# Optimization experiments

Hardware: AMD Instinct MI355X
Metric: run time of the kernel (lower is better)

The kernel has to match this reference:

```python
import jax, jax.numpy as jnp
import numpy as np

B, L, D, H = 2, 2048, 2048, 16
HD = D // H  # 128, must be even for RoPE


def rope(x, seq_len, theta=10000.0):
    """Apply RoPE to x of shape [B, H, L, Dh]."""
    d = x.shape[-1]
    freqs = 1.0 / theta ** (jnp.arange(0, d, 2, dtype=x.dtype) / d)  # [d/2]
    t = jnp.arange(seq_len, dtype=x.dtype)
    f = jnp.outer(t, freqs)                      # [L, d/2]
    sin = jnp.repeat(jnp.sin(f), 2, axis=-1)     # [L, d]
    cos = jnp.repeat(jnp.cos(f), 2, axis=-1)
    x1, x2 = x[..., ::2], x[..., 1::2]
    x_rot = jnp.stack([-x2, x1], axis=-1).reshape(x.shape)
    return x * cos + x_rot * sin


def setup_inputs() -> dict:
    key = jax.random.key(0)
    k1, k2, k3 = jax.random.split(key, 3)
    x = jax.random.normal(k1, (B, L, D), dtype=jnp.float32)
    w_qkv = jax.random.normal(k2, (D, 3 * D), dtype=jnp.float32) * (1.0 / np.sqrt(D))
    w_proj = jax.random.normal(k3, (D, D), dtype=jnp.float32) * (1.0 / np.sqrt(D))
    return {"x": x, "w_qkv": w_qkv, "w_proj": w_proj}


def reference(x, w_qkv, w_proj):
    Bc, Lc, Dc = x.shape
    scale = 1.0 / np.sqrt(HD)
    qkv = (x @ w_qkv).reshape(Bc, Lc, 3, H, HD)
    q, k, v = qkv[:, :, 0], qkv[:, :, 1], qkv[:, :, 2]   # [B, L, H, Dh]
    # transpose to [B, H, L, Dh], then RoPE (position axis = L)
    q = rope(jnp.transpose(q, (0, 2, 1, 3)), Lc)
    k = rope(jnp.transpose(k, (0, 2, 1, 3)), Lc)
    v = jnp.transpose(v, (0, 2, 1, 3))
    att = jnp.einsum("bhqd,bhkd->bhqk", q, k) * scale   # [B, H, L, L]
    att = jax.nn.softmax(att, axis=-1)
    out = jnp.einsum("bhqk,bhkd->bhqd", att, v)          # [B, H, L, Dh]
    out = jnp.transpose(out, (0, 2, 1, 3)).reshape(Bc, Lc, Dc)
    return out @ w_proj
```

## Files before the change

### kernel.cpp

```cpp
#include <hip/hip_runtime.h>
#include <hip/hip_bf16.h>
#include <cstdint>

typedef short short8 __attribute__((ext_vector_type(8)));
typedef float f32x4 __attribute__((ext_vector_type(4)));

#define AS1 __attribute__((address_space(1)))
#define AS3 __attribute__((address_space(3)))

static __device__ __forceinline__ void async_cp16(const void* g, void* l) {
  __builtin_amdgcn_global_load_lds((const AS1 unsigned int*)g, (AS3 unsigned int*)l, 16, 0, 0);
}

static __device__ __forceinline__ ushort f2bf(float f) {
  unsigned u = __builtin_bit_cast(unsigned, f);
  u += 0x7fffu + ((u >> 16) & 1u);
  return (ushort)(u >> 16);
}
static __device__ __forceinline__ float bf2f(ushort h) {
  unsigned u = ((unsigned)h) << 16;
  return __builtin_bit_cast(float, u);
}

__global__ void cvt_bf16_kernel(const float* __restrict__ in, ushort* __restrict__ out, int n4) {
  int i = blockIdx.x * blockDim.x + threadIdx.x;
  if (i >= n4) return;
  float4 v = ((const float4*)in)[i];
  ushort4 o;
  o.x = f2bf(v.x); o.y = f2bf(v.y); o.z = f2bf(v.z); o.w = f2bf(v.w);
  ((ushort4*)out)[i] = o;
}

__global__ void transpose_cvt_kernel(const float* __restrict__ in, ushort* __restrict__ out,
                                     int R, int C) {
  __shared__ ushort tile[32][33];
  int c0 = blockIdx.x * 32, r0 = blockIdx.y * 32;
  int tx = threadIdx.x, ty = threadIdx.y;
  for (int j = 0; j < 32; j += 8)
    tile[ty + j][tx] = f2bf(in[(size_t)(r0 + ty + j) * C + c0 + tx]);
  __syncthreads();
  for (int j = 0; j < 32; j += 8)
    out[(size_t)(c0 + ty + j) * R + r0 + tx] = tile[tx][ty + j];
}

__global__ __launch_bounds__(256) void gemm_qkv_kernel(
    const ushort* __restrict__ A, const ushort* __restrict__ Bt,
    ushort* __restrict__ qr, ushort* __restrict__ kr, ushort* __restrict__ vt,
    int K, int N) {
  __shared__ __align__(16) ushort smem[8192];
  ushort* As = smem;
  ushort* Bs = smem + 4096;
  const int tid = threadIdx.x;
  const int wave = tid >> 6, lane = tid & 63;
  const int wr = (wave >> 1) * 64, wc = (wave & 1) * 64;
  const int m0 = blockIdx.y * 128, n0 = blockIdx.x * 128;
  const int l4 = lane >> 2, lb8 = (lane & 3) * 8;
  const int fr = lane & 15, fq8 = (lane >> 4) * 8;

  f32x4 acc[4][4] = {};

  for (int k0 = 0; k0 < K; k0 += 32) {
#pragma unroll
    for (int j = 0; j < 2; ++j) {
      const int r = wave * 32 + j * 16 + l4;
      async_cp16(A + (size_t)(m0 + r) * K + k0 + lb8, As + wave * 1024 + j * 512);
      async_cp16(Bt + (size_t)(n0 + r) * K + k0 + lb8, Bs + wave * 1024 + j * 512);
    }
    __syncthreads();
    short8 af[4], bf_[4];
#pragma unroll
    for (int i = 0; i < 4; ++i) {
      af[i] = *(const short8*)(As + (wr + i * 16 + fr) * 32 + fq8);
      bf_[i] = *(const short8*)(Bs + (wc + i * 16 + fr) * 32 + fq8);
    }
#pragma unroll
    for (int mi = 0; mi < 4; ++mi)
#pragma unroll
      for (int ni = 0; ni < 4; ++ni)
        acc[mi][ni] = __builtin_amdgcn_mfma_f32_16x16x32_bf16(af[mi], bf_[ni], acc[mi][ni], 0, 0, 0);
    __syncthreads();
  }

  const int rq = (lane >> 4) * 4;
  if (n0 >= 4096) {
    ushort* vtile = smem + wave * 1024;
    const int col0 = n0 + wc;
    const int row0 = m0 + wr;
    const int b = row0 >> 11, l0 = row0 & 2047;
    const int swz = (fr & 3) << 4;
#pragma unroll
    for (int ni = 0; ni < 4; ++ni) {
#pragma unroll
      for (int mi = 0; mi < 4; ++mi)
#pragma unroll
        for (int r = 0; r < 4; ++r) {
          int ll = mi * 16 + rq + r;
          vtile[fr * 64 + (ll ^ swz)] = f2bf(acc[mi][ni][r]);
        }
#pragma unroll
      for (int t = 0; t < 2; ++t) {
        int dl = t * 8 + (lane >> 3);
        int l8 = (lane & 7) * 8;
        int lsw = l8 ^ ((dl & 3) << 4);
        int rem = (col0 + ni * 16 + dl) & 2047;
        int h = rem >> 7, dh = rem & 127;
        *(short8*)(vt + ((size_t)((b << 4) + h) * 128 + dh) * 2048 + l0 + l8) =
            *(const short8*)(vtile + dl * 64 + lsw);
      }
    }
  } else {
    ushort* dst = (n0 >= 2048) ? kr : qr;
#pragma unroll
    for (int mi = 0; mi < 4; ++mi)
#pragma unroll
      for (int ni = 0; ni < 4; ++ni) {
        int col = n0 + wc + ni * 16 + fr;
        int rem = col & 2047, h = rem >> 7, dh = rem & 127;
#pragma unroll
        for (int r = 0; r < 4; ++r) {
          int row = m0 + wr + mi * 16 + rq + r;
          int b = row >> 11, l = row & 2047;
          dst[((size_t)((b << 4) + h) * 2048 + l) * 128 + dh] = f2bf(acc[mi][ni][r]);
        }
      }
  }
}

__global__ __launch_bounds__(256) void gemm_out_kernel(
    const ushort* __restrict__ A, const ushort* __restrict__ Bt,
    float* __restrict__ C, int K, int N) {
  __shared__ __align__(16) ushort As[128 * 32];
  __shared__ __align__(16) ushort Bs[128 * 32];
  const int tid = threadIdx.x;
  const int wave = tid >> 6, lane = tid & 63;
  const int wr = (wave >> 1) * 64, wc = (wave & 1) * 64;
  const int m0 = blockIdx.y * 128, n0 = blockIdx.x * 128;
  const int l4 = lane >> 2, lb8 = (lane & 3) * 8;
  const int fr = lane & 15, fq8 = (lane >> 4) * 8;

  f32x4 acc[4][4] = {};

  for (int k0 = 0; k0 < K; k0 += 32) {
#pragma unroll
    for (int j = 0; j < 2; ++j) {
      const int r = wave * 32 + j * 16 + l4;
      async_cp16(A + (size_t)(m0 + r) * K + k0 + lb8, As + wave * 1024 + j * 512);
      async_cp16(Bt + (size_t)(n0 + r) * K + k0 + lb8, Bs + wave * 1024 + j * 512);
    }
    __syncthreads();
    short8 af[4], bf_[4];
#pragma unroll
    for (int i = 0; i < 4; ++i) {
      af[i] = *(const short8*)(As + (wr + i * 16 + fr) * 32 + fq8);
      bf_[i] = *(const short8*)(Bs + (wc + i * 16 + fr) * 32 + fq8);
    }
#pragma unroll
    for (int mi = 0; mi < 4; ++mi)
#pragma unroll
      for (int ni = 0; ni < 4; ++ni)
        acc[mi][ni] = __builtin_amdgcn_mfma_f32_16x16x32_bf16(af[mi], bf_[ni], acc[mi][ni], 0, 0, 0);
    __syncthreads();
  }

  const int rq = (lane >> 4) * 4;
#pragma unroll
  for (int mi = 0; mi < 4; ++mi)
#pragma unroll
    for (int ni = 0; ni < 4; ++ni) {
      int col = n0 + wc + ni * 16 + fr;
#pragma unroll
      for (int r = 0; r < 4; ++r) {
        int row = m0 + wr + mi * 16 + rq + r;
        C[(size_t)row * N + col] = acc[mi][ni][r];
      }
    }
}

__global__ void rope_kernel(ushort* __restrict__ q, ushort* __restrict__ k) {
  int idx = blockIdx.x * 256 + threadIdx.x;
  int i = idx & 63;
  int l = (idx >> 6) & 2047;
  int bh = idx >> 17;
  float inv = __builtin_amdgcn_exp2f(-(float)i * (13.287712379549449f / 64.0f));
  float f = (float)l * inv;
  float s, c;
  sincosf(f, &s, &c);
  size_t base = ((size_t)bh * 2048 + l) * 128 + 2 * i;
  float q0 = bf2f(q[base]), q1 = bf2f(q[base + 1]);
  q[base] = f2bf(q0 * c - q1 * s);
  q[base + 1] = f2bf(q1 * c + q0 * s);
  float k0 = bf2f(k[base]), k1 = bf2f(k[base + 1]);
  k[base] = f2bf(k0 * c - k1 * s);
  k[base + 1] = f2bf(k1 * c + k0 * s);
}

__global__ __launch_bounds__(512, 4) void flash_kernel(
    const ushort* __restrict__ qr, const ushort* __restrict__ kr,
    const ushort* __restrict__ vtg, ushort* __restrict__ att) {
  __shared__ __align__(16) ushort Ks[64 * 136];
  __shared__ __align__(16) ushort Vt[128 * 68];
  __shared__ __align__(16) ushort Ps[8 * 16 * 68];

  const int tid = threadIdx.x;
  const int wave = tid >> 6, lane = tid & 63;
  const int qt = blockIdx.x & 15;
  const int bh = blockIdx.x >> 4;
  const int q0 = qt * 128 + wave * 16;
  const size_t bh_base = (size_t)bh * 2048 * 128;

  const int fr = lane & 15;
  const int fq = lane >> 4;
  const float cs = 0.08838834764831845f * 1.4426950408889634f;

  short8 qf[4];
  {
    const ushort* qp = qr + bh_base + (size_t)(q0 + fr) * 128 + fq * 8;
#pragma unroll
    for (int kc = 0; kc < 4; ++kc) qf[kc] = *(const short8*)(qp + kc * 32);
  }

  f32x4 oacc[8];
#pragma unroll
  for (int i = 0; i < 8; ++i) oacc[i] = (f32x4){0.f, 0.f, 0.f, 0.f};
  float l_r[4] = {0.f, 0.f, 0.f, 0.f};

  const int krow = tid >> 3;
  const int kc8 = tid & 7;
  const int vrow = tid >> 2;
  const int vc8 = tid & 3;

  ushort* pw = &Ps[wave * 16 * 68];

  short8 kpre[2], vpre[2];
  {
    const ushort* kg = kr + bh_base + (size_t)krow * 128;
    const ushort* vg = vtg + bh_base + (size_t)vrow * 2048;
#pragma unroll
    for (int i = 0; i < 2; ++i) {
      kpre[i] = *(const short8*)(kg + (kc8 + 8 * i) * 8);
      vpre[i] = *(const short8*)(vg + (vc8 + 4 * i) * 8);
    }
  }

  for (int kt = 0; kt < 32; ++kt) {
    __syncthreads();
#pragma unroll
    for (int i = 0; i < 2; ++i) {
      *(short8*)(&Ks[krow * 136 + (kc8 + 8 * i) * 8]) = kpre[i];
      *(short8*)(&Vt[vrow * 68 + (vc8 + 4 * i) * 8]) = vpre[i];
    }
    __syncthreads();
    if (kt < 31) {
      const ushort* kg = kr + bh_base + (size_t)((kt + 1) * 64 + krow) * 128;
      const ushort* vg = vtg + bh_base + (size_t)vrow * 2048 + (kt + 1) * 64;
#pragma unroll
      for (int i = 0; i < 2; ++i) {
        kpre[i] = *(const short8*)(kg + (kc8 + 8 * i) * 8);
        vpre[i] = *(const short8*)(vg + (vc8 + 4 * i) * 8);
      }
    }

    float sv[4][4];
#pragma unroll
    for (int nt = 0; nt < 4; ++nt) {
      f32x4 a = (f32x4){0.f, 0.f, 0.f, 0.f};
#pragma unroll
      for (int kc = 0; kc < 4; ++kc) {
        short8 kf = *(const short8*)(&Ks[(nt * 16 + fr) * 136 + kc * 32 + fq * 8]);
        a = __builtin_amdgcn_mfma_f32_16x16x32_bf16(qf[kc], kf, a, 0, 0, 0);
      }
#pragma unroll
      for (int r = 0; r < 4; ++r) sv[nt][r] = a[r];
    }

#pragma unroll
    for (int nt = 0; nt < 4; ++nt)
#pragma unroll
      for (int r = 0; r < 4; ++r) {
        float pv = __builtin_amdgcn_exp2f(sv[nt][r] * cs);
        l_r[r] += pv;
        pw[(fq * 4 + r) * 68 + nt * 16 + fr] = f2bf(pv);
      }

#pragma unroll
    for (int kc2 = 0; kc2 < 2; ++kc2) {
      short8 pf = *(const short8*)(&pw[fr * 68 + kc2 * 32 + fq * 8]);
#pragma unroll
      for (int dt = 0; dt < 8; ++dt) {
        short8 vf = *(const short8*)(&Vt[(dt * 16 + fr) * 68 + kc2 * 32 + fq * 8]);
        oacc[dt] = __builtin_amdgcn_mfma_f32_16x16x32_bf16(pf, vf, oacc[dt], 0, 0, 0);
      }
    }
  }

  const int b = bh >> 4, h = bh & 15;
#pragma unroll
  for (int r = 0; r < 4; ++r) {
    float l = l_r[r];
    l += __shfl_xor(l, 1);
    l += __shfl_xor(l, 2);
    l += __shfl_xor(l, 4);
    l += __shfl_xor(l, 8);
    float inv = 1.0f / l;
    size_t row = (size_t)(b * 2048 + q0 + fq * 4 + r) * 2048 + h * 128;
#pragma unroll
    for (int dt = 0; dt < 8; ++dt)
      att[row + dt * 16 + fr] = f2bf(oacc[dt][r] * inv);
  }
}

extern "C" void kernel_launch(void* const* d_in, const int* in_sizes, int n_in,
                              void* d_out, int out_size, void* d_ws, size_t ws_size,
                              hipStream_t stream) {
  const float* x = (const float*)d_in[0];
  const float* w_qkv = (const float*)d_in[1];
  const float* w_proj = (const float*)d_in[2];
  float* out = (float*)d_out;

  char* p = (char*)d_ws;
  ushort* xb = (ushort*)p;  p += (size_t)4096 * 2048 * 2;
  ushort* wqt = (ushort*)p; p += (size_t)6144 * 2048 * 2;
  ushort* wpt = (ushort*)p; p += (size_t)2048 * 2048 * 2;
  ushort* qr = (ushort*)p;  p += (size_t)32 * 2048 * 128 * 2;
  ushort* kr = (ushort*)p;  p += (size_t)32 * 2048 * 128 * 2;
  ushort* vt = (ushort*)p;  p += (size_t)32 * 2048 * 128 * 2;
  ushort* att = (ushort*)p; p += (size_t)4096 * 2048 * 2;

  cvt_bf16_kernel<<<8192, 256, 0, stream>>>(x, xb, 4096 * 2048 / 4);
  transpose_cvt_kernel<<<dim3(192, 64), dim3(32, 8), 0, stream>>>(w_qkv, wqt, 2048, 6144);
  transpose_cvt_kernel<<<dim3(64, 64), dim3(32, 8), 0, stream>>>(w_proj, wpt, 2048, 2048);
  gemm_qkv_kernel<<<dim3(48, 32), 256, 0, stream>>>(xb, wqt, qr, kr, vt, 2048, 6144);
  rope_kernel<<<16384, 256, 0, stream>>>(qr, kr);
  flash_kernel<<<512, 512, 0, stream>>>(qr, kr, vt, att);
  gemm_out_kernel<<<dim3(16, 32), 256, 0, stream>>>(att, wpt, out, 2048, 2048);
}
```

Measured before the change: 462.4 us.

## Rewrite QKV GEMM with 256x256 tiles and double-buffered k64 pipeline

```diff
diff --git a/kernel.cpp b/kernel.cpp
--- a/kernel.cpp
+++ b/kernel.cpp
@@ -21,6 +21,11 @@
   unsigned u = ((unsigned)h) << 16;
   return __builtin_bit_cast(float, u);
 }
+
+#define FENCE asm volatile("" ::: "memory")
+#define BARRIER do { FENCE; __builtin_amdgcn_s_barrier(); FENCE; } while (0)
+#define WAITLGKM asm volatile("s_waitcnt lgkmcnt(0)" ::: "memory")
+#define WAITVM(N) asm volatile("s_waitcnt vmcnt(" #N ")" ::: "memory")
 
 __global__ void cvt_bf16_kernel(const float* __restrict__ in, ushort* __restrict__ out, int n4) {
   int i = blockIdx.x * blockDim.x + threadIdx.x;
@@ -43,84 +48,153 @@
     out[(size_t)(c0 + ty + j) * R + r0 + tx] = tile[tx][ty + j];
 }
 
-__global__ __launch_bounds__(256) void gemm_qkv_kernel(
+__global__ __launch_bounds__(512, 2) void gemm_qkv_kernel(
     const ushort* __restrict__ A, const ushort* __restrict__ Bt,
     ushort* __restrict__ qr, ushort* __restrict__ kr, ushort* __restrict__ vt,
     int K, int N) {
-  __shared__ __align__(16) ushort smem[8192];
-  ushort* As = smem;
-  ushort* Bs = smem + 4096;
+  __shared__ __align__(16) ushort smem[65536];
   const int tid = threadIdx.x;
   const int wave = tid >> 6, lane = tid & 63;
-  const int wr = (wave >> 1) * 64, wc = (wave & 1) * 64;
-  const int m0 = blockIdx.y * 128, n0 = blockIdx.x * 128;
-  const int l4 = lane >> 2, lb8 = (lane & 3) * 8;
-  const int fr = lane & 15, fq8 = (lane >> 4) * 8;
-
-  f32x4 acc[4][4] = {};
-
-  for (int k0 = 0; k0 < K; k0 += 32) {
-#pragma unroll
-    for (int j = 0; j < 2; ++j) {
-      const int r = wave * 32 + j * 16 + l4;
-      async_cp16(A + (size_t)(m0 + r) * K + k0 + lb8, As + wave * 1024 + j * 512);
-      async_cp16(Bt + (size_t)(n0 + r) * K + k0 + lb8, Bs + wave * 1024 + j * 512);
-    }
-    __syncthreads();
-    short8 af[4], bf_[4];
-#pragma unroll
-    for (int i = 0; i < 4; ++i) {
-      af[i] = *(const short8*)(As + (wr + i * 16 + fr) * 32 + fq8);
-      bf_[i] = *(const short8*)(Bs + (wc + i * 16 + fr) * 32 + fq8);
-    }
-#pragma unroll
-    for (int mi = 0; mi < 4; ++mi)
-#pragma unroll
-      for (int ni = 0; ni < 4; ++ni)
-        acc[mi][ni] = __builtin_amdgcn_mfma_f32_16x16x32_bf16(af[mi], bf_[ni], acc[mi][ni], 0, 0, 0);
-    __syncthreads();
-  }
-
-  const int rq = (lane >> 4) * 4;
-  if (n0 >= 4096) {
-    ushort* vtile = smem + wave * 1024;
-    const int col0 = n0 + wc;
-    const int row0 = m0 + wr;
-    const int b = row0 >> 11, l0 = row0 & 2047;
-    const int swz = (fr & 3) << 4;
-#pragma unroll
-    for (int ni = 0; ni < 4; ++ni) {
-#pragma unroll
-      for (int mi = 0; mi < 4; ++mi)
+  const int wm = wave >> 2, wn = wave & 3;
+  const int m0 = blockIdx.y * 256, n0 = blockIdx.x * 256;
+  const int frl = lane & 15, fq = lane >> 4;
+  const int sx = fq ^ (frl & 7);
+  const int srow = tid >> 3;
+  const int slog8 = (((tid & 7) ^ ((tid >> 3) & 7)) << 3);
+
+  const ushort* aG = A + (size_t)(m0 + srow) * K + slog8;
+  const ushort* bG = Bt + (size_t)(n0 + srow) * K + slog8;
+  ushort* lw = smem + wave * 512;
+
+  f32x4 acc[8][4] = {};
+  short8 aF[4][2], bF[2][2][2];
+
+  auto stA = [&](int tt, int h) {
+    ushort* l = lw + (tt & 1) * 32768 + h * 8192;
+    const ushort* g = aG + (size_t)(h * 128) * K + tt * 64;
+    async_cp16(g, l);
+    async_cp16(g + (size_t)64 * K, l + 4096);
+  };
+  auto stB = [&](int tt, int h) {
+    ushort* l = lw + (tt & 1) * 32768 + 16384 + h * 8192;
+    const ushort* g = bG + (size_t)(h * 128) * K + tt * 64;
+    async_cp16(g, l);
+    async_cp16(g + (size_t)64 * K, l + 4096);
+  };
+  auto LDA = [&](int buf, int mh) {
+#pragma unroll
+    for (int mf = 0; mf < 4; ++mf)
+#pragma unroll
+      for (int kk = 0; kk < 2; ++kk)
+        aF[mf][kk] = *(const short8*)(smem + buf * 32768 +
+            (wm * 128 + mh * 64 + mf * 16 + frl) * 64 + ((sx ^ (kk << 2)) << 3));
+  };
+  auto LDB = [&](int buf, int nh) {
+#pragma unroll
+    for (int j = 0; j < 2; ++j)
+#pragma unroll
+      for (int kk = 0; kk < 2; ++kk)
+        bF[nh][j][kk] = *(const short8*)(smem + buf * 32768 + 16384 +
+            (wn * 64 + nh * 32 + j * 16 + frl) * 64 + ((sx ^ (kk << 2)) << 3));
+  };
+  auto MFMAQ = [&](int mh, int nh) {
+    __builtin_amdgcn_s_setprio(1);
+#pragma unroll
+    for (int mf = 0; mf < 4; ++mf)
+#pragma unroll
+      for (int j = 0; j < 2; ++j)
+#pragma unroll
+        for (int kk = 0; kk < 2; ++kk)
+          acc[mh * 4 + mf][nh * 2 + j] = __builtin_amdgcn_mfma_f32_16x16x32_bf16(
+              aF[mf][kk], bF[nh][j][kk], acc[mh * 4 + mf][nh * 2 + j], 0, 0, 0);
+    __builtin_amdgcn_s_setprio(0);
+  };
+
+  stB(0, 0); stB(0, 1); stA(0, 0); stA(0, 1);
+  stB(1, 0); stB(1, 1);
+  WAITVM(4);
+  BARRIER;
+
+  const int NT = K >> 6;
+  for (int i = 0; i < NT / 2 - 1; ++i) {
+    const int t = 2 * i;
+    LDA(0, 0); LDB(0, 0); stA(t + 1, 0);
+    BARRIER; WAITLGKM; MFMAQ(0, 0); BARRIER;
+    LDB(0, 1); stA(t + 1, 1);
+    BARRIER; WAITLGKM; MFMAQ(0, 1); BARRIER;
+    LDA(0, 1); stB(t + 2, 0);
+    BARRIER; WAITLGKM; MFMAQ(1, 0); BARRIER;
+    stB(t + 2, 1);
+    BARRIER; WAITLGKM; MFMAQ(1, 1); WAITVM(4); BARRIER;
+    LDA(1, 0); LDB(1, 0); stA(t + 2, 0);
+    BARRIER; WAITLGKM; MFMAQ(0, 0); BARRIER;
+    LDB(1, 1); stA(t + 2, 1);
+    BARRIER; WAITLGKM; MFMAQ(0, 1); BARRIER;
+    LDA(1, 1); stB(t + 3, 0);
+    BARRIER; WAITLGKM; MFMAQ(1, 0); BARRIER;
+    stB(t + 3, 1);
+    BARRIER; WAITLGKM; MFMAQ(1, 1); WAITVM(4); BARRIER;
+  }
+  {
+    const int t = NT - 2;
+    LDA(0, 0); LDB(0, 0); stA(t + 1, 0);
+    BARRIER; WAITLGKM; MFMAQ(0, 0); BARRIER;
+    LDB(0, 1); stA(t + 1, 1);
+    BARRIER; WAITLGKM; MFMAQ(0, 1); BARRIER;
+    LDA(0, 1);
+    BARRIER; WAITLGKM; MFMAQ(1, 0); BARRIER;
+    BARRIER; WAITLGKM; MFMAQ(1, 1); WAITVM(0); BARRIER;
+    LDA(1, 0); LDB(1, 0);
+    BARRIER; WAITLGKM; MFMAQ(0, 0); BARRIER;
+    LDB(1, 1);
+    BARRIER; WAITLGKM; MFMAQ(0, 1); BARRIER;
+    LDA(1, 1);
+    BARRIER; WAITLGKM; MFMAQ(1, 0); BARRIER;
+    BARRIER; WAITLGKM; MFMAQ(1, 1); BARRIER;
+  }
+
+  const int rq = fq * 4;
+  if (n0 < 4096) {
+    ushort* dst = (n0 >= 2048) ? kr : qr;
+#pragma unroll
+    for (int mi = 0; mi < 8; ++mi)
+#pragma unroll
+      for (int ni = 0; ni < 4; ++ni) {
+        int col = n0 + wn * 64 + ni * 16 + frl;
+        int rem = col & 2047, h = rem >> 7, dh = rem & 127;
 #pragma unroll
         for (int r = 0; r < 4; ++r) {
-          int ll = mi * 16 + rq + r;
-          vtile[fr * 64 + (ll ^ swz)] = f2bf(acc[mi][ni][r]);
-        }
-#pragma unroll
-      for (int t = 0; t < 2; ++t) {
-        int dl = t * 8 + (lane >> 3);
-        int l8 = (lane & 7) * 8;
-        int lsw = l8 ^ ((dl & 3) << 4);
-        int rem = (col0 + ni * 16 + dl) & 2047;
-        int h = rem >> 7, dh = rem & 127;
-        *(short8*)(vt + ((size_t)((b << 4) + h) * 128 + dh) * 2048 + l0 + l8) =
-            *(const short8*)(vtile + dl * 64 + lsw);
-      }
-    }
-  } else {
-    ushort* dst = (n0 >= 2048) ? kr : qr;
-#pragma unroll
-    for (int mi = 0; mi < 4; ++mi)
-#pragma unroll
-      for (int ni = 0; ni < 4; ++ni) {
-        int col = n0 + wc + ni * 16 + fr;
-        int rem = col & 2047, h = rem >> 7, dh = rem & 127;
-#pragma unroll
-        for (int r = 0; r < 4; ++r) {
-          int row = m0 + wr + mi * 16 + rq + r;
+          int row = m0 + wm * 128 + mi * 16 + rq + r;
           int b = row >> 11, l = row & 2047;
           dst[((size_t)((b << 4) + h) * 2048 + l) * 128 + dh] = f2bf(acc[mi][ni][r]);
+        }
+      }
+  } else {
+    ushort* vtile = smem + wave * 1024;
+    const int col0 = n0 + wn * 64;
+    const int row0 = m0 + wm * 128;
+    const int b = row0 >> 11, l0 = row0 & 2047;
+    const int swz = (frl & 3) << 4;
+#pragma unroll
+    for (int hm = 0; hm < 2; ++hm)
+#pragma unroll
+      for (int ni = 0; ni < 4; ++ni) {
+#pragma unroll
+        for (int mi = 0; mi < 4; ++mi)
+#pragma unroll
+          for (int r = 0; r < 4; ++r) {
+            int ll = mi * 16 + rq + r;
+            vtile[frl * 64 + (ll ^ swz)] = f2bf(acc[hm * 4 + mi][ni][r]);
+          }
+#pragma unroll
+        for (int tt = 0; tt < 2; ++tt) {
+          int dl = tt * 8 + (lane >> 3);
+          int l8 = (lane & 7) * 8;
+          int lsw = l8 ^ ((dl & 3) << 4);
+          int rem = (col0 + ni * 16 + dl) & 2047;
+          int h = rem >> 7, dh = rem & 127;
+          *(short8*)(vt + ((size_t)((b << 4) + h) * 128 + dh) * 2048 + l0 + hm * 64 + l8) =
+              *(const short8*)(vtile + dl * 64 + lsw);
         }
       }
   }
@@ -329,7 +403,7 @@
   cvt_bf16_kernel<<<8192, 256, 0, stream>>>(x, xb, 4096 * 2048 / 4);
   transpose_cvt_kernel<<<dim3(192, 64), dim3(32, 8), 0, stream>>>(w_qkv, wqt, 2048, 6144);
   transpose_cvt_kernel<<<dim3(64, 64), dim3(32, 8), 0, stream>>>(w_proj, wpt, 2048, 2048);
-  gemm_qkv_kernel<<<dim3(48, 32), 256, 0, stream>>>(xb, wqt, qr, kr, vt, 2048, 6144);
+  gemm_qkv_kernel<<<dim3(24, 16), 512, 0, stream>>>(xb, wqt, qr, kr, vt, 2048, 6144);
   rope_kernel<<<16384, 256, 0, stream>>>(qr, kr);
   flash_kernel<<<512, 512, 0, stream>>>(qr, kr, vt, att);
   gemm_out_kernel<<<dim3(16, 32), 256, 0, stream>>>(att, wpt, out, 2048, 2048);
```

New measurement: 454.8 us. No clear change (-1.6%).
